# Optimization experiments

Hardware: AMD Instinct MI355X
Metric: run time of the kernel (lower is better)

Reference implementation:

```python
import jax, jax.numpy as jnp
import numpy as np

EPS = 1e-5


def setup_inputs() -> dict:
    key = jax.random.key(0)
    ks = jax.random.split(key, 5)
    B, C, H, W = 64, 512, 28, 28
    G = 8
    c_half = C // (2 * G)  # 32
    return {
        "x": jax.random.normal(ks[0], (B, C, H, W), dtype=jnp.float32),
        "cweight": jax.random.normal(ks[1], (c_half,), dtype=jnp.float32),
        "cbias": jax.random.normal(ks[2], (c_half,), dtype=jnp.float32),
        "sweight": jax.random.normal(ks[3], (c_half,), dtype=jnp.float32),
        "sbias": jax.random.normal(ks[4], (c_half,), dtype=jnp.float32),
        "G": G,
    }


def reference(x, cweight, cbias, sweight, sbias, G):
    B, C, H, W = x.shape
    HW = H * W
    Cg = C // G
    c_half = Cg // 2

    # group view: [B*G, Cg, HW]
    xg = x.reshape(B * G, Cg, HW)
    x0 = xg[:, :c_half]   # channel-attention half
    x1 = xg[:, c_half:]   # spatial-attention half

    # channel attention: sigmoid(cweight * avgpool_hw(x0) + cbias), per channel
    m = jnp.mean(x0, axis=-1, keepdims=True)                    # [BG, c_half, 1]
    a0 = jax.nn.sigmoid(cweight[None, :, None] * m + cbias[None, :, None])
    y0 = x0 * a0

    # spatial attention: GN stats over the whole c_half*HW slab per (b,g)
    mu = jnp.mean(x1, axis=(1, 2), keepdims=True)               # [BG, 1, 1]
    var = jnp.mean(x1 * x1, axis=(1, 2), keepdims=True) - mu * mu
    rstd = jax.lax.rsqrt(jnp.maximum(var, 0.0) + EPS)
    norm = (x1 - mu) * rstd
    a1 = jax.nn.sigmoid(sweight[None, :, None] * norm + sbias[None, :, None])
    y1 = x1 * a1

    y = jnp.concatenate([y0, y1], axis=1).reshape(B, C, HW)

    # channel shuffle with 2 groups: out[:, 2*w + g2] = y[:, g2*(C//2) + w]
    y = y.reshape(B, 2, C // 2, HW).transpose(0, 2, 1, 3).reshape(B, C, H, W)
    return y
```

## Files before the change

kernel.cpp:

```cpp
#include <hip/hip_runtime.h>

#define EPSV 1e-5f

__device__ __forceinline__ float sigmoidf_(float z) {
    return 1.0f / (1.0f + __expf(-z));
}

__global__ __launch_bounds__(1024, 4) void fused_sgate_kernel(
    const float* __restrict__ x,
    const float* __restrict__ cweight,
    const float* __restrict__ cbias,
    const float* __restrict__ sweight,
    const float* __restrict__ sbias,
    float* __restrict__ out)
{
    constexpr int HW = 784;
    constexpr int CG = 64;
    constexpr int NELEM = CG * HW;

    const int bg  = blockIdx.x;
    const int b   = bg >> 3;
    const int g   = bg & 7;
    const int tid = threadIdx.x;
    const int cc  = tid >> 4;
    const int ts  = tid & 15;

    const float4* __restrict__ xch =
        (const float4*)(x + (size_t)bg * NELEM + (size_t)cc * HW);

    float4 v[13];
#pragma unroll
    for (int k = 0; k < 12; ++k) v[k] = xch[ts + 16 * k];
    const bool extra = (ts < 4);
    v[12] = make_float4(0.f, 0.f, 0.f, 0.f);
    if (extra) v[12] = xch[192 + ts];

    float s = 0.f, ss = 0.f;
#pragma unroll
    for (int k = 0; k < 13; ++k) {
        s  += (v[k].x + v[k].y) + (v[k].z + v[k].w);
        ss += (v[k].x * v[k].x + v[k].y * v[k].y)
            + (v[k].z * v[k].z + v[k].w * v[k].w);
    }

#pragma unroll
    for (int m = 8; m >= 1; m >>= 1) {
        s  += __shfl_xor(s,  m, 64);
        ss += __shfl_xor(ss, m, 64);
    }
    const float chan_sum = s;

    s  += __shfl_xor(s, 16, 64);
    s  += __shfl_xor(s, 32, 64);
    ss += __shfl_xor(ss, 16, 64);
    ss += __shfl_xor(ss, 32, 64);

    __shared__ float lds_s[16];
    __shared__ float lds_ss[16];
    __shared__ float lds_stats[2];

    const int w = tid >> 6;
    if ((tid & 63) == 0) { lds_s[w] = s; lds_ss[w] = ss; }
    __syncthreads();
    if (tid == 0) {
        float S = 0.f, SS = 0.f;
#pragma unroll
        for (int i = 8; i < 16; ++i) { S += lds_s[i]; SS += lds_ss[i]; }
        constexpr float inv_n = 1.0f / (32.0f * 784.0f);
        const float mu   = S * inv_n;
        const float var  = SS * inv_n - mu * mu;
        const float rstd = rsqrtf(fmaxf(var, 0.f) + EPSV);
        lds_stats[0] = mu;
        lds_stats[1] = rstd;
    }
    __syncthreads();

    const int c_concat = g * CG + cc;
    const int cp = (c_concat < 256) ? (2 * c_concat)
                                    : (2 * (c_concat - 256) + 1);
    float4* __restrict__ och =
        (float4*)(out + (size_t)b * (512 * HW) + (size_t)cp * HW);

    if (cc < 32) {
        const float mval = chan_sum * (1.0f / 784.0f);
        const float a0 = sigmoidf_(cweight[cc] * mval + cbias[cc]);
#pragma unroll
        for (int k = 0; k < 12; ++k) {
            float4 r;
            r.x = v[k].x * a0; r.y = v[k].y * a0;
            r.z = v[k].z * a0; r.w = v[k].w * a0;
            och[ts + 16 * k] = r;
        }
        if (extra) {
            float4 r;
            r.x = v[12].x * a0; r.y = v[12].y * a0;
            r.z = v[12].z * a0; r.w = v[12].w * a0;
            och[192 + ts] = r;
        }
    } else {
        const float mu   = lds_stats[0];
        const float rstd = lds_stats[1];
        const float wgt  = sweight[cc - 32];
        const float bs   = sbias[cc - 32];
#pragma unroll
        for (int k = 0; k < 12; ++k) {
            float4 r;
            r.x = v[k].x * sigmoidf_(wgt * ((v[k].x - mu) * rstd) + bs);
            r.y = v[k].y * sigmoidf_(wgt * ((v[k].y - mu) * rstd) + bs);
            r.z = v[k].z * sigmoidf_(wgt * ((v[k].z - mu) * rstd) + bs);
            r.w = v[k].w * sigmoidf_(wgt * ((v[k].w - mu) * rstd) + bs);
            och[ts + 16 * k] = r;
        }
        if (extra) {
            float4 r;
            r.x = v[12].x * sigmoidf_(wgt * ((v[12].x - mu) * rstd) + bs);
            r.y = v[12].y * sigmoidf_(wgt * ((v[12].y - mu) * rstd) + bs);
            r.z = v[12].z * sigmoidf_(wgt * ((v[12].z - mu) * rstd) + bs);
            r.w = v[12].w * sigmoidf_(wgt * ((v[12].w - mu) * rstd) + bs);
            och[192 + ts] = r;
        }
    }
}

extern "C" void kernel_launch(void* const* d_in, const int* in_sizes, int n_in,
                              void* d_out, int out_size, void* d_ws, size_t ws_size,
                              hipStream_t stream) {
    const float* x  = (const float*)d_in[0];
    const float* cw = (const float*)d_in[1];
    const float* cb = (const float*)d_in[2];
    const float* sw = (const float*)d_in[3];
    const float* sb = (const float*)d_in[4];
    float* out = (float*)d_out;

    const int B = in_sizes[0] / (512 * 784);
    const int nblocks = B * 8;

    fused_sgate_kernel<<<nblocks, 1024, 0, stream>>>(x, cw, cb, sw, sb, out);
}
```

Measured before the change: 194.3 us.

## Split fused gating kernel into stats pass and grid-stride apply pass

```diff
diff --git a/kernel.cpp b/kernel.cpp
--- a/kernel.cpp
+++ b/kernel.cpp
@@ -6,119 +6,98 @@
     return 1.0f / (1.0f + __expf(-z));
 }
 
-__global__ __launch_bounds__(1024, 4) void fused_sgate_kernel(
-    const float* __restrict__ x,
+__global__ __launch_bounds__(512, 4) void stats_kernel(
+    const float4* __restrict__ x4,
     const float* __restrict__ cweight,
     const float* __restrict__ cbias,
-    const float* __restrict__ sweight,
-    const float* __restrict__ sbias,
-    float* __restrict__ out)
+    float* __restrict__ ws)
 {
-    constexpr int HW = 784;
-    constexpr int CG = 64;
-    constexpr int NELEM = CG * HW;
+    const int bg  = blockIdx.x;
+    const int tid = threadIdx.x;
+    const int cc  = tid >> 3;
+    const int ts  = tid & 7;
 
-    const int bg  = blockIdx.x;
-    const int b   = bg >> 3;
-    const int g   = bg & 7;
-    const int tid = threadIdx.x;
-    const int cc  = tid >> 4;
-    const int ts  = tid & 15;
-
-    const float4* __restrict__ xch =
-        (const float4*)(x + (size_t)bg * NELEM + (size_t)cc * HW);
-
-    float4 v[13];
-#pragma unroll
-    for (int k = 0; k < 12; ++k) v[k] = xch[ts + 16 * k];
-    const bool extra = (ts < 4);
-    v[12] = make_float4(0.f, 0.f, 0.f, 0.f);
-    if (extra) v[12] = xch[192 + ts];
+    const float4* __restrict__ xch = x4 + (size_t)bg * (64 * 196) + cc * 196;
 
     float s = 0.f, ss = 0.f;
 #pragma unroll
-    for (int k = 0; k < 13; ++k) {
-        s  += (v[k].x + v[k].y) + (v[k].z + v[k].w);
-        ss += (v[k].x * v[k].x + v[k].y * v[k].y)
-            + (v[k].z * v[k].z + v[k].w * v[k].w);
+    for (int k = 0; k < 24; ++k) {
+        float4 v = xch[ts + 8 * k];
+        s  += (v.x + v.y) + (v.z + v.w);
+        ss += (v.x * v.x + v.y * v.y) + (v.z * v.z + v.w * v.w);
+    }
+    if (ts < 4) {
+        float4 v = xch[192 + ts];
+        s  += (v.x + v.y) + (v.z + v.w);
+        ss += (v.x * v.x + v.y * v.y) + (v.z * v.z + v.w * v.w);
     }
 
-#pragma unroll
-    for (int m = 8; m >= 1; m >>= 1) {
-        s  += __shfl_xor(s,  m, 64);
-        ss += __shfl_xor(ss, m, 64);
+    s  += __shfl_xor(s, 1, 64);  s  += __shfl_xor(s, 2, 64);  s  += __shfl_xor(s, 4, 64);
+    ss += __shfl_xor(ss, 1, 64); ss += __shfl_xor(ss, 2, 64); ss += __shfl_xor(ss, 4, 64);
+
+    __shared__ float lds_s[4];
+    __shared__ float lds_ss[4];
+
+    if (cc < 32) {
+        if (ts == 0) {
+            const float mean = s * (1.0f / 784.0f);
+            ws[(size_t)bg * 34 + cc] = sigmoidf_(cweight[cc] * mean + cbias[cc]);
+        }
+    } else {
+        s  += __shfl_xor(s, 8, 64);  s  += __shfl_xor(s, 16, 64);  s  += __shfl_xor(s, 32, 64);
+        ss += __shfl_xor(ss, 8, 64); ss += __shfl_xor(ss, 16, 64); ss += __shfl_xor(ss, 32, 64);
+        const int w = (tid >> 6) - 4;
+        if ((tid & 63) == 0) { lds_s[w] = s; lds_ss[w] = ss; }
     }
-    const float chan_sum = s;
-
-    s  += __shfl_xor(s, 16, 64);
-    s  += __shfl_xor(s, 32, 64);
-    ss += __shfl_xor(ss, 16, 64);
-    ss += __shfl_xor(ss, 32, 64);
-
-    __shared__ float lds_s[16];
-    __shared__ float lds_ss[16];
-    __shared__ float lds_stats[2];
-
-    const int w = tid >> 6;
-    if ((tid & 63) == 0) { lds_s[w] = s; lds_ss[w] = ss; }
     __syncthreads();
     if (tid == 0) {
-        float S = 0.f, SS = 0.f;
-#pragma unroll
-        for (int i = 8; i < 16; ++i) { S += lds_s[i]; SS += lds_ss[i]; }
+        const float S  = (lds_s[0] + lds_s[1]) + (lds_s[2] + lds_s[3]);
+        const float SS = (lds_ss[0] + lds_ss[1]) + (lds_ss[2] + lds_ss[3]);
         constexpr float inv_n = 1.0f / (32.0f * 784.0f);
         const float mu   = S * inv_n;
         const float var  = SS * inv_n - mu * mu;
         const float rstd = rsqrtf(fmaxf(var, 0.f) + EPSV);
-        lds_stats[0] = mu;
-        lds_stats[1] = rstd;
+        ws[(size_t)bg * 34 + 32] = mu;
+        ws[(size_t)bg * 34 + 33] = rstd;
     }
-    __syncthreads();
+}
 
-    const int c_concat = g * CG + cc;
-    const int cp = (c_concat < 256) ? (2 * c_concat)
-                                    : (2 * (c_concat - 256) + 1);
-    float4* __restrict__ och =
-        (float4*)(out + (size_t)b * (512 * HW) + (size_t)cp * HW);
+__global__ __launch_bounds__(256, 8) void apply_kernel(
+    const float4* __restrict__ x4,
+    const float* __restrict__ sweight,
+    const float* __restrict__ sbias,
+    const float* __restrict__ ws,
+    float4* __restrict__ out4,
+    int total4)
+{
+    for (int i = blockIdx.x * 256 + threadIdx.x; i < total4;
+         i += gridDim.x * 256) {
+        const int bg  = i / 12544;
+        const int rem = i - bg * 12544;
+        const int cc  = rem / 196;
+        const int p   = rem - cc * 196;
 
-    if (cc < 32) {
-        const float mval = chan_sum * (1.0f / 784.0f);
-        const float a0 = sigmoidf_(cweight[cc] * mval + cbias[cc]);
-#pragma unroll
-        for (int k = 0; k < 12; ++k) {
-            float4 r;
-            r.x = v[k].x * a0; r.y = v[k].y * a0;
-            r.z = v[k].z * a0; r.w = v[k].w * a0;
-            och[ts + 16 * k] = r;
+        const float4 v = x4[i];
+        float4 r;
+        if (cc < 32) {
+            const float a0 = ws[(size_t)bg * 34 + cc];
+            r.x = v.x * a0; r.y = v.y * a0; r.z = v.z * a0; r.w = v.w * a0;
+        } else {
+            const float mu   = ws[(size_t)bg * 34 + 32];
+            const float rstd = ws[(size_t)bg * 34 + 33];
+            const float w    = sweight[cc - 32];
+            const float bch  = sbias[cc - 32];
+            r.x = v.x * sigmoidf_(w * ((v.x - mu) * rstd) + bch);
+            r.y = v.y * sigmoidf_(w * ((v.y - mu) * rstd) + bch);
+            r.z = v.z * sigmoidf_(w * ((v.z - mu) * rstd) + bch);
+            r.w = v.w * sigmoidf_(w * ((v.w - mu) * rstd) + bch);
         }
-        if (extra) {
-            float4 r;
-            r.x = v[12].x * a0; r.y = v[12].y * a0;
-            r.z = v[12].z * a0; r.w = v[12].w * a0;
-            och[192 + ts] = r;
-        }
-    } else {
-        const float mu   = lds_stats[0];
-        const float rstd = lds_stats[1];
-        const float wgt  = sweight[cc - 32];
-        const float bs   = sbias[cc - 32];
-#pragma unroll
-        for (int k = 0; k < 12; ++k) {
-            float4 r;
-            r.x = v[k].x * sigmoidf_(wgt * ((v[k].x - mu) * rstd) + bs);
-            r.y = v[k].y * sigmoidf_(wgt * ((v[k].y - mu) * rstd) + bs);
-            r.z = v[k].z * sigmoidf_(wgt * ((v[k].z - mu) * rstd) + bs);
-            r.w = v[k].w * sigmoidf_(wgt * ((v[k].w - mu) * rstd) + bs);
-            och[ts + 16 * k] = r;
-        }
-        if (extra) {
-            float4 r;
-            r.x = v[12].x * sigmoidf_(wgt * ((v[12].x - mu) * rstd) + bs);
-            r.y = v[12].y * sigmoidf_(wgt * ((v[12].y - mu) * rstd) + bs);
-            r.z = v[12].z * sigmoidf_(wgt * ((v[12].z - mu) * rstd) + bs);
-            r.w = v[12].w * sigmoidf_(wgt * ((v[12].w - mu) * rstd) + bs);
-            och[192 + ts] = r;
-        }
+
+        const int b  = bg >> 3;
+        const int g  = bg & 7;
+        const int c  = g * 64 + cc;
+        const int cp = (c < 256) ? (2 * c) : (2 * (c - 256) + 1);
+        out4[(size_t)b * 100352 + (size_t)cp * 196 + p] = r;
     }
 }
 
@@ -131,9 +110,16 @@
     const float* sw = (const float*)d_in[3];
     const float* sb = (const float*)d_in[4];
     float* out = (float*)d_out;
+    float* ws  = (float*)d_ws;
 
     const int B = in_sizes[0] / (512 * 784);
-    const int nblocks = B * 8;
+    const int nbg = B * 8;
+    const int total4 = B * 512 * 196;
 
-    fused_sgate_kernel<<<nblocks, 1024, 0, stream>>>(x, cw, cb, sw, sb, out);
+    stats_kernel<<<nbg, 512, 0, stream>>>(
+        (const float4*)x, cw, cb, ws);
+
+    const int apply_blocks = 2048;
+    apply_kernel<<<apply_blocks, 256, 0, stream>>>(
+        (const float4*)x, sw, sb, ws, (float4*)out, total4);
 }
```

Result: slower. 204.9 us (+5.4%).
